# Kernel tuning notes

Hardware: AMD Instinct MI355X
Metric: run time of the kernel (lower is better)

Reference implementation:

```python
import jax, jax.numpy as jnp
import numpy as np

IN_DIM = 256
QK_DIM = IN_DIM // 8


def setup_inputs() -> dict:
    key = jax.random.key(0)
    ks = jax.random.split(key, 10)
    B, C, W, H = 4, IN_DIM, 64, 64
    a = jax.random.normal(ks[0], (B, C, W, H), dtype=jnp.float32)
    b = jax.random.normal(ks[1], (B, C, W, H), dtype=jnp.float32)
    c = jax.random.uniform(ks[2], (B, 1, 2 * W, 2 * H), dtype=jnp.float32)
    scale = 0.02
    wq = jax.random.normal(ks[3], (QK_DIM, C), dtype=jnp.float32) * scale
    bq = jnp.zeros((QK_DIM,), dtype=jnp.float32)
    wk = jax.random.normal(ks[4], (QK_DIM, C), dtype=jnp.float32) * scale
    bk = jnp.zeros((QK_DIM,), dtype=jnp.float32)
    wv = jax.random.normal(ks[5], (C, C), dtype=jnp.float32) * scale
    bv = jnp.zeros((C,), dtype=jnp.float32)
    gamma = jnp.ones((1,), dtype=jnp.float32)
    return {"a": a, "b": b, "c": c, "wq": wq, "bq": bq, "wk": wk,
            "bk": bk, "wv": wv, "bv": bv, "gamma": gamma}


def reference(a, b, c, wq, bq, wk, bk, wv, bv, gamma):
    B, C, W, H = a.shape
    N = W * H
    # F.interpolate(c, scale_factor=1/down_rate, mode='nearest'): output idx i -> input idx i*down_rate
    down = c.shape[2] // W
    cd = c[:, :, ::down, ::down]                      # [B,1,W,H]
    # 1x1 convs as channel contractions
    q = jnp.einsum('bchw,oc->bohw', a, wq) + bq[None, :, None, None]
    k = jnp.einsum('bchw,oc->bohw', b, wk) + bk[None, :, None, None]
    v = jnp.einsum('bchw,oc->bohw', a, wv) + bv[None, :, None, None]
    qf = q.reshape(B, QK_DIM, N)                      # proj_query^T rows are spatial
    kf = k.reshape(B, QK_DIM, N)
    vf = v.reshape(B, C, N)
    sim = jnp.einsum('bdi,bdj->bij', qf, kf)          # [B,N,N]
    cflat = cd.reshape(B, N)
    # mask[b,i,j] = cflat[b,i] (per-query multiplicative logit scaling)
    logits = sim * cflat[:, :, None]
    attn = jax.nn.softmax(logits, axis=-1)            # [B,N,N]
    out_attn = jnp.einsum('bcj,bij->bci', vf, attn).reshape(B, C, W, H)
    out = gamma * a * cd + (1.0 - cd) * out_attn
    return out
```

## Files before the change

### kernel.cpp

```cpp
#include <hip/hip_runtime.h>

#define LOG2E 1.44269504088896340736f

typedef __attribute__((ext_vector_type(8))) short short8;
typedef __attribute__((ext_vector_type(4))) float float4v;
typedef __attribute__((ext_vector_type(2))) float float2v;
typedef __attribute__((ext_vector_type(2))) int int2v;

__device__ inline unsigned short f2bf(float f) {
    union { float f; unsigned u; } v; v.f = f;
    unsigned r = v.u + 0x7fffu + ((v.u >> 16) & 1u);
    return (unsigned short)(r >> 16);
}
__device__ inline float bf2f(unsigned short u) {
    union { unsigned u; float f; } v; v.u = ((unsigned)u) << 16;
    return v.f;
}
__device__ inline unsigned pk_bf16(float a, float b) {
    union { float f; unsigned u; } ua, ub; ua.f = a; ub.f = b;
    return __builtin_amdgcn_perm(ub.u + 0x8000u, ua.u + 0x8000u, 0x07060302u);
}

__global__ void wcvt_kernel(const float* __restrict__ wq, const float* __restrict__ wk,
                            const float* __restrict__ wv, unsigned short* __restrict__ Wbf)
{
    int idx = blockIdx.x * 256 + threadIdx.x;
    int e4  = idx * 4;
    int row = e4 >> 8, col = e4 & 255;
    const float* src = (row < 32) ? (wq + row * 256 + col)
                     : (row < 64) ? (wk + (row - 32) * 256 + col)
                                  : (wv + (row - 64) * 256 + col);
    float4v v = *(const float4v*)src;
    int2v p;
    p.x = (unsigned)f2bf(v[0]) | ((unsigned)f2bf(v[1]) << 16);
    p.y = (unsigned)f2bf(v[2]) | ((unsigned)f2bf(v[3]) << 16);
    *(int2v*)(Wbf + e4) = p;
}

__launch_bounds__(256, 3)
__global__ void proj_kernel(const float* __restrict__ a_p, const float* __restrict__ b_p,
                            const float* __restrict__ c_p,
                            const float* __restrict__ bq, const float* __restrict__ bk,
                            const float* __restrict__ bv,
                            const unsigned short* __restrict__ Wbf,
                            unsigned short* __restrict__ Qg, unsigned short* __restrict__ Kg,
                            unsigned short* __restrict__ Vg)
{
    __shared__ unsigned At[16 * 132];
    __shared__ unsigned Bt[16 * 132];

    const int t    = threadIdx.x;
    const int blk  = blockIdx.x;
    const int b    = blk & 3;
    const int t16  = blk >> 2;
    const int i0   = t16 * 16;
    const int lane = t & 63;
    const int w    = t >> 6;
    const int q    = lane >> 4;
    const int n    = lane & 15;

    {
        int arr = t >> 7, p = t & 127;
        const float* src = (arr ? b_p : a_p) + ((size_t)(b * 256 + 2 * p)) * 4096 + i0;
        unsigned* dst = arr ? Bt : At;
        float4v r0[4], r1[4];
#pragma unroll
        for (int j4 = 0; j4 < 4; ++j4) r0[j4] = *(const float4v*)(src + j4 * 4);
#pragma unroll
        for (int j4 = 0; j4 < 4; ++j4) r1[j4] = *(const float4v*)(src + 4096 + j4 * 4);
#pragma unroll
        for (int j4 = 0; j4 < 4; ++j4)
#pragma unroll
            for (int jj = 0; jj < 4; ++jj) {
                int i = j4 * 4 + jj;
                dst[i * 132 + p] = (unsigned)f2bf(r0[j4][jj]) | ((unsigned)f2bf(r1[j4][jj]) << 16);
            }
    }
    __syncthreads();

    float4v acc[5];
#pragma unroll
    for (int kk = 0; kk < 5; ++kk) acc[kk] = (float4v){0.f, 0.f, 0.f, 0.f};

#pragma unroll
    for (int kc = 0; kc < 8; ++kc) {
        short8 atf = *(const short8*)((const unsigned short*)At + n * 264 + kc * 32 + q * 8);
        short8 btf = atf;
        if (w >= 2)
            btf = *(const short8*)((const unsigned short*)Bt + n * 264 + kc * 32 + q * 8);
#pragma unroll
        for (int kk = 0; kk < 5; ++kk) {
            int mt = w + 4 * kk;
            short8 wf = *(const short8*)(Wbf + (size_t)(mt * 16 + n) * 256 + kc * 32 + q * 8);
            short8 bsel = (mt == 2 || mt == 3) ? btf : atf;
            acc[kk] = __builtin_amdgcn_mfma_f32_16x16x32_bf16(wf, bsel, acc[kk], 0, 0, 0);
        }
    }

    const int i = i0 + n;
    const int jj = i & 31;
    const int pperm = ((jj & 15) >> 2) * 8 + (jj >> 4) * 4 + (jj & 3);
    const float cdq = c_p[b * 16384 + (i >> 6) * 256 + (i & 63) * 2] * LOG2E;
#pragma unroll
    for (int kk = 0; kk < 5; ++kk) {
        int mt = w + 4 * kk;
#pragma unroll
        for (int r = 0; r < 4; ++r) {
            int mm = mt * 16 + q * 4 + r;
            float bias = (mm < 32) ? bq[mm] : (mm < 64) ? bk[mm - 32] : bv[mm - 64];
            float val = acc[kk][r] + bias;
            if (mm < 32) {
                Qg[(size_t)(b * 4096 + i) * 32 + mm] = f2bf(val * cdq);
            } else if (mm < 64) {
                Kg[(size_t)(b * 4096 + i) * 32 + (mm - 32)] = f2bf(val);
            } else {
                Vg[(size_t)(((b * 128 + (i >> 5)) * 256) + (mm - 64)) * 32 + pperm] = f2bf(val);
            }
        }
    }
}

__launch_bounds__(256, 3)
__global__ void attn_kernel(const unsigned short* __restrict__ Qg,
                            const unsigned short* __restrict__ Kg,
                            const unsigned short* __restrict__ Vg,
                            unsigned short* __restrict__ Opart, float* __restrict__ lsum)
{
    const int t    = threadIdx.x;
    const int blk  = blockIdx.x;
    const int b    = blk & 3;
    const int rt   = (blk >> 2) & 63;
    const int s    = blk >> 8;
    const int i0   = rt * 64;
    const int lane = t & 63;
    const int w    = t >> 6;
    const int q    = lane >> 4;
    const int n    = lane & 15;

    short8 qf[4];
#pragma unroll
    for (int ig = 0; ig < 4; ++ig)
        qf[ig] = *(const short8*)(Qg + (size_t)(b * 4096 + i0 + ig * 16 + n) * 32 + q * 8);

    float4v acc[4][4];
#pragma unroll
    for (int ig = 0; ig < 4; ++ig)
#pragma unroll
        for (int ct = 0; ct < 4; ++ct) acc[ig][ct] = (float4v){0.f, 0.f, 0.f, 0.f};
    float lsc[4] = {0.f, 0.f, 0.f, 0.f};

    const float4v m16v = (float4v){-16.f, -16.f, -16.f, -16.f};

    const unsigned short* kb = Kg + (size_t)(b * 4096 + s * 1024 + n) * 32 + q * 8;
    const unsigned short* vb = Vg + ((size_t)((b * 128 + s * 32) * 256 + w * 64 + n)) * 32 + q * 8;

    short8 kf0 = *(const short8*)(kb);
    short8 kf1 = *(const short8*)(kb + 512);

#pragma unroll 1
    for (int it = 0; it < 32; ++it) {
        short8 vf[4];
#pragma unroll
        for (int ct = 0; ct < 4; ++ct)
            vf[ct] = *(const short8*)(vb + ct * 512);

        short8 pf[4];
#pragma unroll
        for (int ig = 0; ig < 4; ++ig) {
            float4v s0 = __builtin_amdgcn_mfma_f32_16x16x32_bf16(kf0, qf[ig], m16v, 0, 0, 0);
            float4v s1 = __builtin_amdgcn_mfma_f32_16x16x32_bf16(kf1, qf[ig], m16v, 0, 0, 0);
            float p0 = __builtin_amdgcn_exp2f(s0[0]), p1 = __builtin_amdgcn_exp2f(s0[1]);
            float p2 = __builtin_amdgcn_exp2f(s0[2]), p3 = __builtin_amdgcn_exp2f(s0[3]);
            float p4 = __builtin_amdgcn_exp2f(s1[0]), p5 = __builtin_amdgcn_exp2f(s1[1]);
            float p6 = __builtin_amdgcn_exp2f(s1[2]), p7 = __builtin_amdgcn_exp2f(s1[3]);
            lsc[ig] += ((p0 + p1) + (p2 + p3)) + ((p4 + p5) + (p6 + p7));
            union { short8 s8; unsigned u[4]; } pf_;
            pf_.u[0] = pk_bf16(p0, p1);
            pf_.u[1] = pk_bf16(p2, p3);
            pf_.u[2] = pk_bf16(p4, p5);
            pf_.u[3] = pk_bf16(p6, p7);
            pf[ig] = pf_.s8;
        }

        kf0 = *(const short8*)(kb + 1024);
        kf1 = *(const short8*)(kb + 1536);

#pragma unroll
        for (int ig = 0; ig < 4; ++ig)
#pragma unroll
            for (int ct = 0; ct < 4; ++ct)
                acc[ig][ct] = __builtin_amdgcn_mfma_f32_16x16x32_bf16(pf[ig], vf[ct], acc[ig][ct], 0, 0, 0);

        kb += 1024;
        vb += 8192;
    }

    const size_t obase = (size_t)blk * 16384;
#pragma unroll
    for (int ig = 0; ig < 4; ++ig)
#pragma unroll
        for (int ct = 0; ct < 4; ++ct) {
            int c = w * 64 + ct * 16 + n;
            int i = ig * 16 + q * 4;
            int2v pk;
            pk.x = (int)pk_bf16(acc[ig][ct][0], acc[ig][ct][1]);
            pk.y = (int)pk_bf16(acc[ig][ct][2], acc[ig][ct][3]);
            *(int2v*)(Opart + obase + (size_t)c * 64 + i) = pk;
        }
#pragma unroll
    for (int ig = 0; ig < 4; ++ig) {
        float v = lsc[ig];
        v += __shfl_xor(v, 16, 64);
        v += __shfl_xor(v, 32, 64);
        if (w == 0 && lane < 16)
            lsum[(size_t)blk * 64 + ig * 16 + lane] = v;
    }
}

__launch_bounds__(256, 4)
__global__ void combine_kernel(const float* __restrict__ a_p, const float* __restrict__ c_p,
                               const float* __restrict__ gamma_p,
                               const unsigned short* __restrict__ Opart,
                               const float* __restrict__ lsum, float* __restrict__ out)
{
    __shared__ float invL[64];
    __shared__ float cdl[64];

    const int t   = threadIdx.x;
    const int blk = blockIdx.x;
    const int b   = blk & 3;
    const int rt  = (blk >> 2) & 63;
    const int cs  = blk >> 8;
    const int i0  = rt * 64;

    if (t < 64) {
        float L = 0.f;
#pragma unroll
        for (int s = 0; s < 4; ++s)
            L += lsum[(size_t)((s << 8) | (rt << 2) | b) * 64 + t];
        invL[t] = 1.0f / L;
        cdl[t] = c_p[b * 16384 + rt * 256 + 2 * t];
    }
    __syncthreads();

    const float gam = gamma_p[0];
    const int il = (t & 31) * 2;
    const int cq = t >> 5;
#pragma unroll
    for (int k = 0; k < 4; ++k) {
        int c = cs * 32 + cq + 8 * k;
        float o0 = 0.f, o1 = 0.f;
#pragma unroll
        for (int s = 0; s < 4; ++s) {
            int idx = (s << 8) | (rt << 2) | b;
            unsigned pr = *(const unsigned*)(Opart + (size_t)idx * 16384 + (size_t)c * 64 + il);
            o0 += bf2f((unsigned short)(pr & 0xffff));
            o1 += bf2f((unsigned short)(pr >> 16));
        }
        o0 *= invL[il];
        o1 *= invL[il + 1];
        size_t gi = (size_t)(b * 256 + c) * 4096 + i0 + il;
        float2v av = *(const float2v*)(a_p + gi);
        float cd0 = cdl[il], cd1 = cdl[il + 1];
        float2v ov;
        ov[0] = gam * av[0] * cd0 + (1.0f - cd0) * o0;
        ov[1] = gam * av[1] * cd1 + (1.0f - cd1) * o1;
        *(float2v*)(out + gi) = ov;
    }
}

extern "C" void kernel_launch(void* const* d_in, const int* in_sizes, int n_in,
                              void* d_out, int out_size, void* d_ws, size_t ws_size,
                              hipStream_t stream)
{
    const float* a_p   = (const float*)d_in[0];
    const float* b_p   = (const float*)d_in[1];
    const float* c_p   = (const float*)d_in[2];
    const float* wq    = (const float*)d_in[3];
    const float* bq    = (const float*)d_in[4];
    const float* wk    = (const float*)d_in[5];
    const float* bk    = (const float*)d_in[6];
    const float* wv    = (const float*)d_in[7];
    const float* bv    = (const float*)d_in[8];
    const float* gamma = (const float*)d_in[9];
    float* out = (float*)d_out;

    unsigned short* Qg    = (unsigned short*)d_ws;
    unsigned short* Kg    = Qg + (size_t)4 * 4096 * 32;
    unsigned short* Vg    = Kg + (size_t)4 * 4096 * 32;
    unsigned short* Wbf   = Vg + (size_t)4 * 256 * 4096;
    unsigned short* Opart = Wbf + (size_t)320 * 256;
    float*          lsum  = (float*)(Opart + (size_t)1024 * 16384);

    wcvt_kernel<<<80, 256, 0, stream>>>(wq, wk, wv, Wbf);
    proj_kernel<<<1024, 256, 0, stream>>>(a_p, b_p, c_p, bq, bk, bv, Wbf, Qg, Kg, Vg);
    attn_kernel<<<1024, 256, 0, stream>>>(Qg, Kg, Vg, Opart, lsum);
    combine_kernel<<<2048, 256, 0, stream>>>(a_p, c_p, gamma, Opart, lsum, out);
}
```

Baseline: 195.4 us.

## Split attention waves over row halves and channel halves to cut redundant exp work

Each wave in the attention kernel now handles 32 query rows and 128 value channels instead of 64 rows and 64 channels. This halves the per-wave QK score MFMAs and exp2 evaluations, which were duplicated across all four waves, while doubling the V fragment loads per iteration. The projection kernel's global-load/LDS-store staging is regrouped into halves and its k-loop unroll is reduced to 2, likely to ease register pressure.

```diff
diff --git a/kernel.cpp b/kernel.cpp
--- a/kernel.cpp
+++ b/kernel.cpp
@@ -62,19 +62,20 @@
     {
         int arr = t >> 7, p = t & 127;
         const float* src = (arr ? b_p : a_p) + ((size_t)(b * 256 + 2 * p)) * 4096 + i0;
-        unsigned* dst = arr ? Bt : At;
-        float4v r0[4], r1[4];
-#pragma unroll
-        for (int j4 = 0; j4 < 4; ++j4) r0[j4] = *(const float4v*)(src + j4 * 4);
-#pragma unroll
-        for (int j4 = 0; j4 < 4; ++j4) r1[j4] = *(const float4v*)(src + 4096 + j4 * 4);
-#pragma unroll
-        for (int j4 = 0; j4 < 4; ++j4)
-#pragma unroll
-            for (int jj = 0; jj < 4; ++jj) {
-                int i = j4 * 4 + jj;
-                dst[i * 132 + p] = (unsigned)f2bf(r0[j4][jj]) | ((unsigned)f2bf(r1[j4][jj]) << 16);
-            }
+        unsigned* dst = (arr ? Bt : At) + p;
+#pragma unroll
+        for (int h = 0; h < 2; ++h) {
+            float4v r0a = *(const float4v*)(src + h * 8);
+            float4v r0b = *(const float4v*)(src + h * 8 + 4);
+            float4v r1a = *(const float4v*)(src + 4096 + h * 8);
+            float4v r1b = *(const float4v*)(src + 4096 + h * 8 + 4);
+#pragma unroll
+            for (int jj = 0; jj < 4; ++jj)
+                dst[(h * 8 + jj) * 132] = (unsigned)f2bf(r0a[jj]) | ((unsigned)f2bf(r1a[jj]) << 16);
+#pragma unroll
+            for (int jj = 0; jj < 4; ++jj)
+                dst[(h * 8 + 4 + jj) * 132] = (unsigned)f2bf(r0b[jj]) | ((unsigned)f2bf(r1b[jj]) << 16);
+        }
     }
     __syncthreads();
 
@@ -82,7 +83,7 @@
 #pragma unroll
     for (int kk = 0; kk < 5; ++kk) acc[kk] = (float4v){0.f, 0.f, 0.f, 0.f};
 
-#pragma unroll
+#pragma unroll 2
     for (int kc = 0; kc < 8; ++kc) {
         short8 atf = *(const short8*)((const unsigned short*)At + n * 264 + kc * 32 + q * 8);
         short8 btf = atf;
@@ -134,39 +135,41 @@
     const int i0   = rt * 64;
     const int lane = t & 63;
     const int w    = t >> 6;
+    const int rh   = w & 1;
+    const int ch   = w >> 1;
     const int q    = lane >> 4;
     const int n    = lane & 15;
 
-    short8 qf[4];
-#pragma unroll
-    for (int ig = 0; ig < 4; ++ig)
-        qf[ig] = *(const short8*)(Qg + (size_t)(b * 4096 + i0 + ig * 16 + n) * 32 + q * 8);
-
-    float4v acc[4][4];
-#pragma unroll
-    for (int ig = 0; ig < 4; ++ig)
-#pragma unroll
-        for (int ct = 0; ct < 4; ++ct) acc[ig][ct] = (float4v){0.f, 0.f, 0.f, 0.f};
-    float lsc[4] = {0.f, 0.f, 0.f, 0.f};
+    short8 qf[2];
+#pragma unroll
+    for (int ig = 0; ig < 2; ++ig)
+        qf[ig] = *(const short8*)(Qg + (size_t)(b * 4096 + i0 + rh * 32 + ig * 16 + n) * 32 + q * 8);
+
+    float4v acc[2][8];
+#pragma unroll
+    for (int ig = 0; ig < 2; ++ig)
+#pragma unroll
+        for (int ct = 0; ct < 8; ++ct) acc[ig][ct] = (float4v){0.f, 0.f, 0.f, 0.f};
+    float lsc[2] = {0.f, 0.f};
 
     const float4v m16v = (float4v){-16.f, -16.f, -16.f, -16.f};
 
     const unsigned short* kb = Kg + (size_t)(b * 4096 + s * 1024 + n) * 32 + q * 8;
-    const unsigned short* vb = Vg + ((size_t)((b * 128 + s * 32) * 256 + w * 64 + n)) * 32 + q * 8;
+    const unsigned short* vb = Vg + ((size_t)((b * 128 + s * 32) * 256 + ch * 128 + n)) * 32 + q * 8;
 
     short8 kf0 = *(const short8*)(kb);
     short8 kf1 = *(const short8*)(kb + 512);
 
 #pragma unroll 1
     for (int it = 0; it < 32; ++it) {
-        short8 vf[4];
-#pragma unroll
-        for (int ct = 0; ct < 4; ++ct)
+        short8 vf[8];
+#pragma unroll
+        for (int ct = 0; ct < 8; ++ct)
             vf[ct] = *(const short8*)(vb + ct * 512);
 
-        short8 pf[4];
-#pragma unroll
-        for (int ig = 0; ig < 4; ++ig) {
+        short8 pf[2];
+#pragma unroll
+        for (int ig = 0; ig < 2; ++ig) {
             float4v s0 = __builtin_amdgcn_mfma_f32_16x16x32_bf16(kf0, qf[ig], m16v, 0, 0, 0);
             float4v s1 = __builtin_amdgcn_mfma_f32_16x16x32_bf16(kf1, qf[ig], m16v, 0, 0, 0);
             float p0 = __builtin_amdgcn_exp2f(s0[0]), p1 = __builtin_amdgcn_exp2f(s0[1]);
@@ -186,9 +189,9 @@
         kf1 = *(const short8*)(kb + 1536);
 
 #pragma unroll
-        for (int ig = 0; ig < 4; ++ig)
-#pragma unroll
-            for (int ct = 0; ct < 4; ++ct)
+        for (int ig = 0; ig < 2; ++ig)
+#pragma unroll
+            for (int ct = 0; ct < 8; ++ct)
                 acc[ig][ct] = __builtin_amdgcn_mfma_f32_16x16x32_bf16(pf[ig], vf[ct], acc[ig][ct], 0, 0, 0);
 
         kb += 1024;
@@ -197,23 +200,23 @@
 
     const size_t obase = (size_t)blk * 16384;
 #pragma unroll
-    for (int ig = 0; ig < 4; ++ig)
-#pragma unroll
-        for (int ct = 0; ct < 4; ++ct) {
-            int c = w * 64 + ct * 16 + n;
-            int i = ig * 16 + q * 4;
+    for (int ig = 0; ig < 2; ++ig)
+#pragma unroll
+        for (int ct = 0; ct < 8; ++ct) {
+            int c = ch * 128 + ct * 16 + n;
+            int i = rh * 32 + ig * 16 + q * 4;
             int2v pk;
             pk.x = (int)pk_bf16(acc[ig][ct][0], acc[ig][ct][1]);
             pk.y = (int)pk_bf16(acc[ig][ct][2], acc[ig][ct][3]);
             *(int2v*)(Opart + obase + (size_t)c * 64 + i) = pk;
         }
 #pragma unroll
-    for (int ig = 0; ig < 4; ++ig) {
+    for (int ig = 0; ig < 2; ++ig) {
         float v = lsc[ig];
         v += __shfl_xor(v, 16, 64);
         v += __shfl_xor(v, 32, 64);
-        if (w == 0 && lane < 16)
-            lsum[(size_t)blk * 64 + ig * 16 + lane] = v;
+        if (ch == 0 && lane < 16)
+            lsum[(size_t)blk * 64 + rh * 32 + ig * 16 + lane] = v;
     }
 }
 
```

New measurement: 228.6 us. 1.17x slower.
